# Kernel optimization log

Measured on AMD Instinct MI355X. Metric: run time of the kernel, lower is better.

The kernel has to match this reference:

```python
import jax, jax.numpy as jnp
import numpy as np

B, T_TREES, LEAVES = 1024, 34, 16
E = 128            # entity = logic = theorem embedding size
N_NF, N_LF = 4, 3  # binary numerical / logic function experts
V_ENT, V_TH = 2000, 32
GT_MAX, ENT_MAX, TH_MAX = 8, 16, 8


def setup_inputs() -> dict:
    key = jax.random.key(0)
    ks = jax.random.split(key, 24)
    s2e = 1.0 / np.sqrt(2 * E)
    s4e = 1.0 / np.sqrt(4 * E)
    se = 1.0 / np.sqrt(E)
    inp = {
        'leaf_idx': jax.random.randint(ks[0], (B, T_TREES, LEAVES), 0, V_ENT),
        'nf_ids':   jax.random.randint(ks[1], (B, T_TREES, 15), 0, N_NF),
        'lf_ids':   jax.random.randint(ks[2], (B, GT_MAX + 1), 0, N_LF),
        'th_idx':   jax.random.randint(ks[3], (B, TH_MAX), 0, V_TH),
        'ent_emb':  jax.random.normal(ks[4], (V_ENT, E)) * 0.02,
        'th_emb':   jax.random.normal(ks[5], (V_TH, E)) * 0.02,
        # nf two2one expert MLPs: Linear(2E,2E) -> ReLU -> Linear(2E,E)
        'nf_W1': jax.random.normal(ks[6], (N_NF, 2 * E, 2 * E)) * s2e,
        'nf_b1': jnp.zeros((N_NF, 2 * E)),
        'nf_W2': jax.random.normal(ks[7], (N_NF, 2 * E, E)) * s2e,
        'nf_b2': jnp.zeros((N_NF, E)),
        # lf two2one expert MLPs: Linear(2E,4E) -> ReLU -> Linear(4E,E)
        'lf_W1': jax.random.normal(ks[8], (N_LF, 2 * E, 4 * E)) * s2e,
        'lf_b1': jnp.zeros((N_LF, 4 * E)),
        'lf_W2': jax.random.normal(ks[9], (N_LF, 4 * E, E)) * s4e,
        'lf_b2': jnp.zeros((N_LF, E)),
        # higher attention linears: logic_size -> {entity,entity,theorem} size
        'he_W': jax.random.normal(ks[10], (E, E)) * se, 'he_b': jnp.zeros((E,)),
        'hg_W': jax.random.normal(ks[11], (E, E)) * se, 'hg_b': jnp.zeros((E,)),
        'ht_W': jax.random.normal(ks[12], (E, E)) * se, 'ht_b': jnp.zeros((E,)),
    }
    return inp


def _expert_mlp(x, ids, W1, b1, W2, b2):
    # x: [..., Din], ids: [...] selecting among K experts; masked sum over K (small fixed loop)
    out = jnp.zeros(x.shape[:-1] + (W2.shape[-1],), x.dtype)
    for k in range(W1.shape[0]):
        h = jax.nn.relu(x @ W1[k] + b1[k]) @ W2[k] + b2[k]
        out = out + jnp.where((ids == k)[..., None], h, 0.0)
    return out


def _attend(keys, q):
    # keys: [B, N, D], q: [B, D] -> attentive context [B, D]
    a = jax.nn.softmax(jnp.einsum('bnd,bd->bn', keys, q), axis=-1)
    return jnp.einsum('bn,bnd->bd', a, keys)


def _forward(leaf_idx, nf_ids, lf_ids, th_idx, ent_emb, th_emb,
             nf_W1, nf_b1, nf_W2, nf_b2, lf_W1, lf_b1, lf_W2, lf_b2,
             he_W, he_b, hg_W, hg_b, ht_W, ht_b):
    # leaf entity embedding lookup: [B, 34, 16, E]
    cur = ent_emb[leaf_idx]
    # recursive tree reduction over 4 levels of binary nf MLPs (batched over all nodes)
    off = 0
    for lvl in range(4):
        n = LEAVES >> (lvl + 1)  # nodes at this level: 8,4,2,1
        x = cur.reshape(cur.shape[0], T_TREES, n, 2 * E)  # concat(left,right)
        ids = nf_ids[..., off:off + n]
        off += n
        cur = _expert_mlp(x, ids, nf_W1, nf_b1, nf_W2, nf_b2)
    roots = cur[..., 0, :]                       # [B, 34, E]
    ent = roots[:, :ENT_MAX]                     # [B, 16, E] standalone entities
    pairs = roots[:, ENT_MAX:].reshape(roots.shape[0], GT_MAX + 1, 2 * E)
    stmt = _expert_mlp(pairs, lf_ids, lf_W1, lf_b1, lf_W2, lf_b2)  # [B, 9, E]
    gt = stmt[:, :GT_MAX]                        # [B, 8, E] ground truths
    obj = stmt[:, GT_MAX]                        # [B, E]    objective
    th = th_emb[th_idx]                          # [B, 8, E] theorems
    ent_ctx = _attend(ent, obj @ he_W + he_b)
    gt_ctx = _attend(gt, obj @ hg_W + hg_b)
    th_ctx = _attend(th, obj @ ht_W + ht_b)
    # higher attentive state: 2*L + E + T = 512
    return jnp.concatenate([obj, gt_ctx, ent_ctx, th_ctx], axis=-1)


def reference(leaf_idx, nf_ids, lf_ids, th_idx, ent_emb, th_emb,
              nf_W1, nf_b1, nf_W2, nf_b2, lf_W1, lf_b1, lf_W2, lf_b2,
              he_W, he_b, hg_W, hg_b, ht_W, ht_b):
    return _forward(leaf_idx, nf_ids, lf_ids, th_idx, ent_emb, th_emb,
                    nf_W1, nf_b1, nf_W2, nf_b2, lf_W1, lf_b1, lf_W2, lf_b2,
                    he_W, he_b, hg_W, hg_b, ht_W, ht_b)
```

## Files before the change

### kernel.cpp

```cpp
#include <hip/hip_runtime.h>
#include <math.h>


typedef unsigned short u16;
typedef unsigned int   u32;
typedef unsigned long long u64;
typedef __attribute__((ext_vector_type(8))) short v8s;
typedef __attribute__((ext_vector_type(4))) float f32x4;

__device__ __forceinline__ float b2f(u16 u) { return __uint_as_float(((u32)u) << 16); }
__device__ __forceinline__ u16 f2b(float f) {
  f = (f == f) ? f : 0.f;
  u32 x = __float_as_uint(f);
  u32 r = x + 0x7fffu + ((x >> 16) & 1u);
  return (u16)(r >> 16);
}

__device__ __forceinline__ void g2lds16(const void* g, void* l) {
  __builtin_amdgcn_global_load_lds(
      (const __attribute__((address_space(1))) void*)g,
      (__attribute__((address_space(3))) void*)l, 16, 0, 0);
}

#define NTREE 34816
#define RLEAF 9216

__global__ __launch_bounds__(256) void setup_k(
    const float* __restrict__ s0, const float* __restrict__ s1,
    const float* __restrict__ s2, const float* __restrict__ s3,
    const float* __restrict__ s4,
    u16* __restrict__ d0, u16* __restrict__ d1, u16* __restrict__ d2,
    u16* __restrict__ d3, u16* __restrict__ d4,
    const int* __restrict__ lf, int* __restrict__ leafcnt, int* __restrict__ leafperm,
    const int* __restrict__ nf, int* __restrict__ bh,
    const int CB, const int NB)
{
  __shared__ float tile[16][17];
  __shared__ int lcnt[16];
  const int t = threadIdx.x;
  const int bid = blockIdx.x;

  if (bid < 4840) {
    const int idx0 = bid * 256;
    if (idx0 < 983040) {
      const float* s; u16* d; int tb, estr, O, kt, mt, e;
      int tloc0;
      if (idx0 < 262144)      { s = s0; d = d0; tb = 0;      estr = 65536;  O = 256; }
      else if (idx0 < 393216) { s = s1; d = d1; tb = 262144; estr = 32768;  O = 128; }
      else if (idx0 < 786432) { s = s2; d = d2; tb = 393216; estr = 131072; O = 512; }
      else                    { s = s3; d = d3; tb = 786432; estr = 65536;  O = 128; }
      tloc0 = idx0 - tb;
      const int blk = tloc0 >> 9;
      const int hb  = (tloc0 >> 8) & 1;
      if (idx0 < 262144)      { kt = blk & 7;  mt = (blk >> 3) & 15; e = blk >> 7; }
      else if (idx0 < 393216) { kt = blk & 7;  mt = (blk >> 3) & 7;  e = blk >> 6; }
      else if (idx0 < 786432) { kt = blk & 7;  mt = (blk >> 3) & 31; e = blk >> 8; }
      else                    { kt = blk & 15; mt = (blk >> 4) & 7;  e = blk >> 7; }
      const int o0 = mt * 16;
      const int k0 = kt * 32 + hb * 16;
      tile[t >> 4][t & 15] = s[(size_t)e * estr + (size_t)(k0 + (t >> 4)) * O + o0 + (t & 15)];
      __syncthreads();
      d[tloc0 + t] = f2b(tile[((t >> 7) << 3) + (t & 7)][(t >> 3) & 15]);
    } else {
      int tl = idx0 + t - 983040;
      d4[tl] = f2b(s4[tl]);
    }
  } else if (bid < 4876) {
    const int gid = (bid - 4840) * 256 + t;
    const int id = lf[gid];
    const int lane = t & 63;
    for (int e = 0; e < 3; ++e) {
      u64 m = __ballot(id == e);
      if (!m) continue;
      int leader = __builtin_ctzll(m);
      int bp = 0;
      if (lane == leader) bp = atomicAdd(&leafcnt[e], (int)__popcll(m));
      bp = __shfl(bp, leader);
      if (id == e)
        leafperm[e * RLEAF + bp + (int)__popcll(m & ((1ull << lane) - 1ull))] = gid;
    }
  } else {
    const int hb2 = bid - 4876;
    const int c = hb2 / NB, b = hb2 - c * NB;
    const int bt0 = c * CB;
    int* bhc = bh + (size_t)c * 16 * NB;
    const int gid = b * 256 + t;
    int id = -1, lr = 0, cofs = 12, ioff = 14, shift = 0;
    if (gid < 8 * CB)       { lr = gid;          cofs = 0;  ioff = 0;  shift = 3; }
    else if (gid < 12 * CB) { lr = gid - 8*CB;   cofs = 4;  ioff = 8;  shift = 2; }
    else if (gid < 14 * CB) { lr = gid - 12*CB;  cofs = 8;  ioff = 12; shift = 1; }
    else if (gid < 15 * CB) { lr = gid - 14*CB;  }
    if (gid < 15 * CB) {
      int bt = bt0 + (lr >> shift);
      int n  = lr & ((1 << shift) - 1);
      id = nf[bt * 15 + ioff + n];
    }
    if (t < 16) lcnt[t] = 0;
    __syncthreads();
    const int lane = t & 63;
    #pragma unroll
    for (int e = 0; e < 4; ++e) {
      u64 m = __ballot(id == e);
      if (m && lane == __builtin_ctzll(m))
        atomicAdd(&lcnt[cofs + e], (int)__popcll(m));
    }
    __syncthreads();
    if (t < 16)
      bhc[t * NB + b] = lcnt[t];
  }
}

__global__ __launch_bounds__(1024) void perm_scan_k(
    int* __restrict__ bh, int* __restrict__ cnt, const int nb)
{
  const int c = blockIdx.x;
  int* bhc = bh + (size_t)c * 16 * nb;
  int* cntc = cnt + c * 16;
  const int s = threadIdx.x >> 6;
  const int lane = threadIdx.x & 63;
  int carry = 0;
  for (int b0 = 0; b0 < nb; b0 += 64) {
    const int b = b0 + lane;
    int v = (b < nb) ? bhc[s * nb + b] : 0;
    int x = v;
    #pragma unroll
    for (int d = 1; d < 64; d <<= 1) {
      int y = __shfl_up(x, d);
      if (lane >= d) x += y;
    }
    if (b < nb) bhc[s * nb + b] = carry + x - v;
    carry += __shfl(x, 63);
  }
  if (lane == 0) cntc[s] = carry;
}

__global__ __launch_bounds__(256) void perm_scatter_k(
    const int* __restrict__ nf, const int* __restrict__ bh,
    int* __restrict__ perm, const int CB, const int bt0, const int nb)
{
  const int gid = blockIdx.x * 256 + threadIdx.x;
  int id = -1, lr = 0, rows = CB, cofs = 12, pofs = 56 * CB, ioff = 14, shift = 0;
  if (gid < 8 * CB)       { lr = gid;          rows = 8*CB; cofs = 0;  pofs = 0;      ioff = 0;  shift = 3; }
  else if (gid < 12 * CB) { lr = gid - 8*CB;   rows = 4*CB; cofs = 4;  pofs = 32*CB;  ioff = 8;  shift = 2; }
  else if (gid < 14 * CB) { lr = gid - 12*CB;  rows = 2*CB; cofs = 8;  pofs = 48*CB;  ioff = 12; shift = 1; }
  else if (gid < 15 * CB) { lr = gid - 14*CB;                 }
  if (gid < 15 * CB) {
    int bt = bt0 + (lr >> shift);
    int n  = lr & ((1 << shift) - 1);
    id = nf[bt * 15 + ioff + n];
  }
  __shared__ int wc[4][16];
  const int w = threadIdx.x >> 6, lane = threadIdx.x & 63;
  if (lane < 16) wc[w][lane] = 0;
  __syncthreads();
  u64 msave[4];
  #pragma unroll
  for (int e = 0; e < 4; ++e) {
    u64 m = __ballot(id == e);
    msave[e] = m;
    if (m && lane == __builtin_ctzll(m))
      wc[w][cofs + e] = (int)__popcll(m);
  }
  __syncthreads();
  #pragma unroll
  for (int e = 0; e < 4; ++e) {
    if (id == e) {
      const int slot = cofs + e;
      int base = bh[slot * nb + blockIdx.x];
      #pragma unroll
      for (int w2 = 0; w2 < 3; ++w2)
        if (w2 < w) base += wc[w2][slot];
      perm[pofs + e * rows + base +
           (int)__popcll(msave[e] & ((1ull << lane) - 1ull))] = lr;
    }
  }
}

template<int HID, int NEXP, int MODE, int MR>
__global__ __launch_bounds__(256, 2) void mlp_k(
    const u16* __restrict__ src, const int* __restrict__ lidx,
    const u16* __restrict__ emb,
    const int* __restrict__ perm, const int* __restrict__ cnt,
    const int rows, const int bt0,
    const u16* __restrict__ W1f, const float* __restrict__ b1,
    const u16* __restrict__ W2f, const float* __restrict__ b2,
    u16* __restrict__ dst)
{
  constexpr int NT  = MR / 16;
  constexpr int MT1 = HID / 64;
  constexpr int K2  = HID / 32;
  constexpr int PD1 = (MT1 <= 4) ? 2 : 1;
  constexpr int NB1 = PD1 + 1;
  constexpr int XB  = MR * 512;
  constexpr int HB  = MR * HID * 2;
  constexpr int UB  = XB > HB ? XB : HB;
  __shared__ __align__(16) char uni[UB];
  __shared__ int rid[MR], soff[2 * MR];
  u16* const xs = (u16*)uni;
  u16* const hs = (u16*)uni;

  int bin = -1, tile = 0, cb = 0;
  {
    int rem = blockIdx.x;
    #pragma unroll
    for (int e = 0; e < NEXP; ++e) {
      int ce = cnt[e];
      int tt = (ce + MR - 1) / MR;
      if (bin < 0) {
        if (rem < tt) { bin = e; tile = rem; cb = ce; }
        else rem -= tt;
      }
    }
  }
  if (bin < 0) return;
  const int rbase = tile * MR;
  const int tid = threadIdx.x;
  const int w  = tid >> 6;
  const int lane = tid & 63;
  const int lm = lane & 15;
  const int lq = lane >> 4;

  const u16* const W1b = W1f + ((size_t)(bin * (HID / 16) + w * MT1) << 12) + lane * 8;
  const u16* const W2b = W2f + ((size_t)((bin * 8 + w * 2) * K2) << 9) + lane * 8;

  v8s afb[NB1][MT1];
  #pragma unroll
  for (int d = 0; d < PD1; ++d)
    #pragma unroll
    for (int m = 0; m < MT1; ++m)
      afb[d][m] = *(const v8s*)(W1b + (size_t)(m * 8 + d) * 512);

  if (tid < MR) {
    int rl = rbase + tid;
    int rlc = rl < cb ? rl : (cb - 1);
    rlc = rlc < 0 ? 0 : rlc;
    int rc = perm[(size_t)bin * rows + rlc];
    rc = rc < 0 ? 0 : (rc >= rows ? rows - 1 : rc);
    rid[tid] = (rl < cb) ? rc : -1;
    if (MODE == 0) {
      int bt = bt0 + (rc >> 3), node = rc & 7;
      int ia = lidx[bt * 16 + node * 2];
      int ib = lidx[bt * 16 + node * 2 + 1];
      ia = ia < 0 ? 0 : (ia > 1999 ? 1999 : ia);
      ib = ib < 0 ? 0 : (ib > 1999 ? 1999 : ib);
      soff[2 * tid]     = ia * 256;
      soff[2 * tid + 1] = ib * 256;
    } else {
      int base;
      if (MODE == 1) base = rc * 512;
      else { int bq = rc / 9, g = rc - bq * 9; base = (bq * 34 + 16 + 2 * g) * 256; }
      soff[2 * tid]     = base;
      soff[2 * tid + 1] = base + 256;
    }
  }
  __syncthreads();

  const char* const sb = (MODE == 0) ? (const char*)emb : (const char*)src;
  #pragma unroll
  for (int i = 0; i < MR / 8; ++i) {
    int d = i * 256 + tid;
    int r = d >> 5, c32d = d & 31;
    int cS = c32d ^ ((r & 7) << 1);
    const char* ga = sb + (size_t)(u32)soff[2 * r + (cS >> 4)] + (cS & 15) * 16;
    char* la = uni + ((size_t)(i * 256 + (tid & 192)) << 4);
    g2lds16(ga, la);
  }
  __syncthreads();

  int rdn[NT];
  #pragma unroll
  for (int n = 0; n < NT; ++n) rdn[n] = rid[n * 16 + lm];

  f32x4 acc[MT1][NT];
  #pragma unroll
  for (int m = 0; m < MT1; ++m)
    #pragma unroll
    for (int n = 0; n < NT; ++n)
      acc[m][n] = f32x4{0.f, 0.f, 0.f, 0.f};

  v8s bfr2[2][NT];
  #pragma unroll
  for (int n = 0; n < NT; ++n) {
    int r = n * 16 + lm;
    int cs = lq ^ ((lm & 7) << 1);
    bfr2[0][n] = *(const v8s*)(xs + r * 256 + cs * 8);
  }
  #pragma unroll
  for (int k = 0; k < 8; ++k) {
    const int cur = k % NB1;
    if (k + PD1 < 8) {
      const int nx = (k + PD1) % NB1;
      #pragma unroll
      for (int m = 0; m < MT1; ++m)
        afb[nx][m] = *(const v8s*)(W1b + (size_t)(m * 8 + k + PD1) * 512);
    }
    const int cb_ = k & 1;
    if (k < 7) {
      #pragma unroll
      for (int n = 0; n < NT; ++n) {
        int r = n * 16 + lm;
        int cs = ((k + 1) * 4 + lq) ^ ((lm & 7) << 1);
        bfr2[cb_ ^ 1][n] = *(const v8s*)(xs + r * 256 + cs * 8);
      }
    }
    __builtin_amdgcn_s_setprio(1);
    #pragma unroll
    for (int m = 0; m < MT1; ++m)
      #pragma unroll
      for (int n = 0; n < NT; ++n)
        acc[m][n] = __builtin_amdgcn_mfma_f32_16x16x32_bf16(afb[cur][m], bfr2[cb_][n], acc[m][n], 0, 0, 0);
    __builtin_amdgcn_s_setprio(0);
  }

  v8s afb2[3][2];
  #pragma unroll
  for (int m = 0; m < 2; ++m)
    afb2[0][m] = *(const v8s*)(W2b + (size_t)(m * K2) * 512);
  #pragma unroll
  for (int m = 0; m < 2; ++m)
    afb2[1][m] = *(const v8s*)(W2b + (size_t)(m * K2 + 1) * 512);

  __syncthreads();

  const float* b1b = b1 + bin * HID;
  #pragma unroll
  for (int m = 0; m < MT1; ++m) {
    const int f = (w * MT1 + m) * 16 + lq * 4;
    float bb0 = b1b[f], bb1 = b1b[f + 1], bb2 = b1b[f + 2], bb3 = b1b[f + 3];
    #pragma unroll
    for (int n = 0; n < NT; ++n) {
      union { u16 h[4]; uint2 v; } pk;
      f32x4 a = acc[m][n];
      pk.h[0] = f2b(fmaxf(a.x + bb0, 0.f));
      pk.h[1] = f2b(fmaxf(a.y + bb1, 0.f));
      pk.h[2] = f2b(fmaxf(a.z + bb2, 0.f));
      pk.h[3] = f2b(fmaxf(a.w + bb3, 0.f));
      int r = n * 16 + lm;
      int cs = (f >> 3) ^ ((lm & 7) << 1);
      *(uint2*)(uni + (size_t)r * (HID * 2) + (cs << 4) + (f & 7) * 2) = pk.v;
    }
  }
  __syncthreads();

  f32x4 acc2[2][NT];
  #pragma unroll
  for (int m = 0; m < 2; ++m)
    #pragma unroll
    for (int n = 0; n < NT; ++n)
      acc2[m][n] = f32x4{0.f, 0.f, 0.f, 0.f};

  #pragma unroll
  for (int n = 0; n < NT; ++n) {
    int r = n * 16 + lm;
    int cs = lq ^ ((lm & 7) << 1);
    bfr2[0][n] = *(const v8s*)(hs + (size_t)r * HID + cs * 8);
  }
  #pragma unroll
  for (int k = 0; k < K2; ++k) {
    const int cur = k % 3;
    if (k < K2 - 2) {
      const int nx2 = (k + 2) % 3;
      #pragma unroll
      for (int m = 0; m < 2; ++m)
        afb2[nx2][m] = *(const v8s*)(W2b + (size_t)(m * K2 + k + 2) * 512);
    }
    const int cb_ = k & 1;
    if (k < K2 - 1) {
      #pragma unroll
      for (int n = 0; n < NT; ++n) {
        int r = n * 16 + lm;
        int cs = ((k + 1) * 4 + lq) ^ ((lm & 7) << 1);
        bfr2[cb_ ^ 1][n] = *(const v8s*)(hs + (size_t)r * HID + cs * 8);
      }
    }
    __builtin_amdgcn_s_setprio(1);
    #pragma unroll
    for (int m = 0; m < 2; ++m)
      #pragma unroll
      for (int n = 0; n < NT; ++n)
        acc2[m][n] = __builtin_amdgcn_mfma_f32_16x16x32_bf16(afb2[cur][m], bfr2[cb_][n], acc2[m][n], 0, 0, 0);
    __builtin_amdgcn_s_setprio(0);
  }

  __syncthreads();
  const float* b2b = b2 + bin * 128;
  #pragma unroll
  for (int m = 0; m < 2; ++m) {
    const int f = (w * 2 + m) * 16 + lq * 4;
    float bb0 = b2b[f], bb1 = b2b[f + 1], bb2 = b2b[f + 2], bb3 = b2b[f + 3];
    #pragma unroll
    for (int n = 0; n < NT; ++n) {
      union { u16 h[4]; uint2 v; } pk;
      f32x4 a = acc2[m][n];
      pk.h[0] = f2b(a.x + bb0);
      pk.h[1] = f2b(a.y + bb1);
      pk.h[2] = f2b(a.z + bb2);
      pk.h[3] = f2b(a.w + bb3);
      int r = n * 16 + lm;
      int c = (w * 2 + m) * 2 + (lq >> 1);
      int cs = c ^ ((lm & 7) << 1);
      *(uint2*)(uni + r * 256 + cs * 16 + (lq & 1) * 8) = pk.v;
    }
  }
  __syncthreads();
  #pragma unroll
  for (int i = 0; i < MR / 16; ++i) {
    int cg = i * 256 + tid;
    int r = cg >> 4, sub = cg & 15;
    int rg = rid[r];
    if (rg >= 0) {
      uint4 v = *(const uint4*)(uni + r * 256 + ((sub ^ ((r & 7) << 1)) << 4));
      *(uint4*)((char*)dst + (size_t)rg * 256 + sub * 16) = v;
    }
  }
}

__global__ __launch_bounds__(128) void attn_k(
    const u16* __restrict__ stmt, const u16* __restrict__ roots,
    const float* __restrict__ themb, const int* __restrict__ thidx,
    const float* __restrict__ wHe, const float* __restrict__ bHe,
    const float* __restrict__ wHg, const float* __restrict__ bHg,
    const float* __restrict__ wHt, const float* __restrict__ bHt,
    float* __restrict__ out)
{
  const int b = blockIdx.x, t = threadIdx.x;
  __shared__ float obj_s[128], q_s[128], keys_s[16 * 132], a_s[16];

  const float obj = b2f(stmt[((size_t)b * 9 + 8) * 128 + t]);
  obj_s[t] = obj;
  out[(size_t)b * 512 + t] = obj;
  __syncthreads();

  for (int a = 0; a < 3; ++a) {
    int cntk;
    const float *Wt, *bv;
    if (a == 0) {
      cntk = 8; Wt = wHg; bv = bHg;
      for (int j = 0; j < 8; ++j)
        keys_s[j * 132 + t] = b2f(stmt[((size_t)b * 9 + j) * 128 + t]);
    } else if (a == 1) {
      cntk = 16; Wt = wHe; bv = bHe;
      for (int j = 0; j < 16; ++j)
        keys_s[j * 132 + t] = b2f(roots[((size_t)b * 34 + j) * 128 + t]);
    } else {
      cntk = 8; Wt = wHt; bv = bHt;
      for (int j = 0; j < 8; ++j) {
        int ti = thidx[b * 8 + j] & 31;
        keys_s[j * 132 + t] = themb[(size_t)ti * 128 + t];
      }
    }
    float q0 = 0.f, q1 = 0.f, q2 = 0.f, q3 = 0.f;
    #pragma unroll 4
    for (int k = 0; k < 128; k += 4) {
      q0 += obj_s[k]     * Wt[(k)     * 128 + t];
      q1 += obj_s[k + 1] * Wt[(k + 1) * 128 + t];
      q2 += obj_s[k + 2] * Wt[(k + 2) * 128 + t];
      q3 += obj_s[k + 3] * Wt[(k + 3) * 128 + t];
    }
    float qa = bv[t] + ((q0 + q1) + (q2 + q3));
    q_s[t] = (qa == qa) ? qa : 0.f;
    __syncthreads();
    {
      int j = t >> 3, s = t & 7;
      if (j < cntk) {
        float sc = 0.f;
        #pragma unroll
        for (int k = 0; k < 16; ++k)
          sc += keys_s[j * 132 + s * 16 + k] * q_s[s * 16 + k];
        sc += __shfl_xor(sc, 1);
        sc += __shfl_xor(sc, 2);
        sc += __shfl_xor(sc, 4);
        if (s == 0) a_s[j] = (sc == sc) ? sc : 0.f;
      }
    }
    __syncthreads();
    if (t < 16) {
      float v = (t < cntk) ? a_s[t] : -3.0e38f;
      float mx = v;
      #pragma unroll
      for (int d = 1; d < 16; d <<= 1) mx = fmaxf(mx, __shfl_xor(mx, d));
      float e = (t < cntk) ? expf(v - mx) : 0.f;
      float sm = e;
      #pragma unroll
      for (int d = 1; d < 16; d <<= 1) sm += __shfl_xor(sm, d);
      if (t < cntk) a_s[t] = e / sm;
    }
    __syncthreads();
    float c = 0.f;
    for (int j = 0; j < cntk; ++j) c += a_s[j] * keys_s[j * 132 + t];
    out[(size_t)b * 512 + 128 * (a + 1) + t] = c;
    __syncthreads();
  }
}

extern "C" void kernel_launch(void* const* d_in, const int* in_sizes, int n_in,
                              void* d_out, int out_size, void* d_ws, size_t ws_size,
                              hipStream_t stream)
{
  const int*   leaf_idx = (const int*)d_in[0];
  const int*   nf_ids   = (const int*)d_in[1];
  const int*   lf_ids   = (const int*)d_in[2];
  const int*   th_idx   = (const int*)d_in[3];
  const float* ent_emb  = (const float*)d_in[4];
  const float* th_emb   = (const float*)d_in[5];
  const float* nf_W1 = (const float*)d_in[6];
  const float* nf_b1 = (const float*)d_in[7];
  const float* nf_W2 = (const float*)d_in[8];
  const float* nf_b2 = (const float*)d_in[9];
  const float* lf_W1 = (const float*)d_in[10];
  const float* lf_b1 = (const float*)d_in[11];
  const float* lf_W2 = (const float*)d_in[12];
  const float* lf_b2 = (const float*)d_in[13];
  const float* he_W = (const float*)d_in[14];
  const float* he_b = (const float*)d_in[15];
  const float* hg_W = (const float*)d_in[16];
  const float* hg_b = (const float*)d_in[17];
  const float* ht_W = (const float*)d_in[18];
  const float* ht_b = (const float*)d_in[19];

  int CB = NTREE;
  while (CB > 544 && 14700000ull + (unsigned long long)CB * 3320ull > (unsigned long long)ws_size)
    CB >>= 1;
  const int nch = NTREE / CB;
  const int NB = (15 * CB + 255) / 256;

  char* ws = (char*)d_ws;
  size_t off = 0;
  auto take = [&](size_t bytes) -> char* {
    char* p = ws + off;
    off = (off + bytes + 255) & ~(size_t)255;
    return p;
  };
  int* cnt      = (int*)take(8192);
  int* leafperm = (int*)take((size_t)3 * RLEAF * 4);
  int* chperm   = (int*)take((size_t)60 * CB * 4);
  int* bh       = (int*)take((size_t)nch * 16 * NB * 4);
  u16* wN1  = (u16*)take((size_t)4 * 256 * 256 * 2);
  u16* wN2  = (u16*)take((size_t)4 * 128 * 256 * 2);
  u16* wL1  = (u16*)take((size_t)3 * 512 * 256 * 2);
  u16* wL2  = (u16*)take((size_t)3 * 128 * 512 * 2);
  u16* embB = (u16*)take((size_t)2000 * 128 * 2);
  u16* bufA  = (u16*)take((size_t)CB * 8 * 128 * 2);
  u16* bufB  = (u16*)take((size_t)CB * 4 * 128 * 2);
  u16* roots = (u16*)take((size_t)NTREE * 128 * 2);
  u16* stmt  = (u16*)take((size_t)RLEAF * 128 * 2);

  int* leafcnt = cnt + nch * 16;

  hipMemsetAsync(leafcnt, 0, 8 * 4, stream);
  setup_k<<<4876 + nch * NB, 256, 0, stream>>>(
      nf_W1, nf_W2, lf_W1, lf_W2, ent_emb, wN1, wN2, wL1, wL2, embB,
      lf_ids, leafcnt, leafperm, nf_ids, bh, CB, NB);
  perm_scan_k<<<nch, 1024, 0, stream>>>(bh, cnt, NB);

  for (int c = 0; c < nch; ++c) {
    const int bt0 = c * CB;
    int* ccnt = cnt + c * 16;
    perm_scatter_k<<<NB, 256, 0, stream>>>(nf_ids, bh + (size_t)c * 16 * NB,
                                           chperm, CB, bt0, NB);
    mlp_k<256, 4, 0, 96><<<(8 * CB + 95) / 96 + 4, 256, 0, stream>>>(
        nullptr, leaf_idx, embB, chperm, ccnt, 8 * CB, bt0,
        wN1, nf_b1, wN2, nf_b2, bufA);
    mlp_k<256, 4, 1, 96><<<(4 * CB + 95) / 96 + 4, 256, 0, stream>>>(
        bufA, nullptr, nullptr, chperm + 32 * CB, ccnt + 4, 4 * CB, 0,
        wN1, nf_b1, wN2, nf_b2, bufB);
    mlp_k<256, 4, 1, 64><<<(2 * CB + 63) / 64 + 4, 256, 0, stream>>>(
        bufB, nullptr, nullptr, chperm + 48 * CB, ccnt + 8, 2 * CB, 0,
        wN1, nf_b1, wN2, nf_b2, bufA);
    mlp_k<256, 4, 1, 64><<<(CB + 63) / 64 + 4, 256, 0, stream>>>(
        bufA, nullptr, nullptr, chperm + 56 * CB, ccnt + 12, CB, 0,
        wN1, nf_b1, wN2, nf_b2, roots + (size_t)bt0 * 128);
  }

  mlp_k<512, 3, 2, 32><<<RLEAF / 32 + 3, 256, 0, stream>>>(
      roots, nullptr, nullptr, leafperm, leafcnt, RLEAF, 0,
      wL1, lf_b1, wL2, lf_b2, stmt);

  attn_k<<<1024, 128, 0, stream>>>(stmt, roots, th_emb, th_idx,
                                   he_W, he_b, hg_W, hg_b, ht_W, ht_b,
                                   (float*)d_out);
}
```

Before: 296.8 us.

## Fuse scatter, tree MLP levels, logic MLP and attention into persistent kernel

Replaces the per-chunk sequence of scatter, four tree-level MLP launches, the logic MLP and the attention launch with one persistent kernel. Blocks loop over virtual block indices and synchronise through a hierarchical atomic grid barrier in workspace memory. The aim is to remove the launch gaps and tail idling between many small dependent kernels. In exchange it relies on every block being co-resident, costs spin-wait overhead at each barrier, and fixes LDS usage at the largest stage's size, which may lower occupancy.

```diff
diff --git a/kernel.cpp b/kernel.cpp
--- a/kernel.cpp
+++ b/kernel.cpp
@@ -20,6 +20,33 @@
   __builtin_amdgcn_global_load_lds(
       (const __attribute__((address_space(1))) void*)g,
       (__attribute__((address_space(3))) void*)l, 16, 0, 0);
+}
+
+__device__ __forceinline__ void gbar(int* gb, int nblk) {
+  __syncthreads();
+  if (threadIdx.x == 0) {
+    __threadfence();
+    int g = __hip_atomic_load(gb + 272, __ATOMIC_ACQUIRE, __HIP_MEMORY_SCOPE_AGENT);
+    const int grp = blockIdx.x & 15;
+    const int gsz = (nblk >> 4) + (grp < (nblk & 15) ? 1 : 0);
+    int a = __hip_atomic_fetch_add(gb + grp * 16, 1, __ATOMIC_ACQ_REL, __HIP_MEMORY_SCOPE_AGENT);
+    if (a == gsz - 1) {
+      __hip_atomic_store(gb + grp * 16, 0, __ATOMIC_RELAXED, __HIP_MEMORY_SCOPE_AGENT);
+      int r = __hip_atomic_fetch_add(gb + 256, 1, __ATOMIC_ACQ_REL, __HIP_MEMORY_SCOPE_AGENT);
+      if (r == 15) {
+        __hip_atomic_store(gb + 256, 0, __ATOMIC_RELAXED, __HIP_MEMORY_SCOPE_AGENT);
+        __hip_atomic_fetch_add(gb + 272, 1, __ATOMIC_RELEASE, __HIP_MEMORY_SCOPE_AGENT);
+      } else {
+        while (__hip_atomic_load(gb + 272, __ATOMIC_ACQUIRE, __HIP_MEMORY_SCOPE_AGENT) == g)
+          __builtin_amdgcn_s_sleep(16);
+      }
+    } else {
+      while (__hip_atomic_load(gb + 272, __ATOMIC_ACQUIRE, __HIP_MEMORY_SCOPE_AGENT) == g)
+        __builtin_amdgcn_s_sleep(16);
+    }
+    __threadfence();
+  }
+  __syncthreads();
 }
 
 #define NTREE 34816
@@ -134,24 +161,25 @@
   if (lane == 0) cntc[s] = carry;
 }
 
-__global__ __launch_bounds__(256) void perm_scatter_k(
-    const int* __restrict__ nf, const int* __restrict__ bh,
-    int* __restrict__ perm, const int CB, const int bt0, const int nb)
+
+__device__ void scatter_body(int vb, const int* __restrict__ nf,
+    const int* __restrict__ bh, int* __restrict__ perm,
+    const int CB, const int bt0, const int nb, int* wc)
 {
-  const int gid = blockIdx.x * 256 + threadIdx.x;
+  __syncthreads();
+  const int gid = vb * 256 + threadIdx.x;
   int id = -1, lr = 0, rows = CB, cofs = 12, pofs = 56 * CB, ioff = 14, shift = 0;
   if (gid < 8 * CB)       { lr = gid;          rows = 8*CB; cofs = 0;  pofs = 0;      ioff = 0;  shift = 3; }
   else if (gid < 12 * CB) { lr = gid - 8*CB;   rows = 4*CB; cofs = 4;  pofs = 32*CB;  ioff = 8;  shift = 2; }
   else if (gid < 14 * CB) { lr = gid - 12*CB;  rows = 2*CB; cofs = 8;  pofs = 48*CB;  ioff = 12; shift = 1; }
-  else if (gid < 15 * CB) { lr = gid - 14*CB;                 }
+  else if (gid < 15 * CB) { lr = gid - 14*CB;  }
   if (gid < 15 * CB) {
     int bt = bt0 + (lr >> shift);
     int n  = lr & ((1 << shift) - 1);
     id = nf[bt * 15 + ioff + n];
   }
-  __shared__ int wc[4][16];
   const int w = threadIdx.x >> 6, lane = threadIdx.x & 63;
-  if (lane < 16) wc[w][lane] = 0;
+  if (lane < 16) wc[w * 16 + lane] = 0;
   __syncthreads();
   u64 msave[4];
   #pragma unroll
@@ -159,17 +187,17 @@
     u64 m = __ballot(id == e);
     msave[e] = m;
     if (m && lane == __builtin_ctzll(m))
-      wc[w][cofs + e] = (int)__popcll(m);
+      wc[w * 16 + cofs + e] = (int)__popcll(m);
   }
   __syncthreads();
   #pragma unroll
   for (int e = 0; e < 4; ++e) {
     if (id == e) {
       const int slot = cofs + e;
-      int base = bh[slot * nb + blockIdx.x];
+      int base = bh[slot * nb + vb];
       #pragma unroll
       for (int w2 = 0; w2 < 3; ++w2)
-        if (w2 < w) base += wc[w2][slot];
+        if (w2 < w) base += wc[w2 * 16 + slot];
       perm[pofs + e * rows + base +
            (int)__popcll(msave[e] & ((1ull << lane) - 1ull))] = lr;
     }
@@ -177,31 +205,28 @@
 }
 
 template<int HID, int NEXP, int MODE, int MR>
-__global__ __launch_bounds__(256, 2) void mlp_k(
+__device__ void mlp_body(int vb,
     const u16* __restrict__ src, const int* __restrict__ lidx,
     const u16* __restrict__ emb,
     const int* __restrict__ perm, const int* __restrict__ cnt,
     const int rows, const int bt0,
     const u16* __restrict__ W1f, const float* __restrict__ b1,
     const u16* __restrict__ W2f, const float* __restrict__ b2,
-    u16* __restrict__ dst)
+    u16* __restrict__ dst, char* uni, int* rid, int* soff)
 {
   constexpr int NT  = MR / 16;
   constexpr int MT1 = HID / 64;
   constexpr int K2  = HID / 32;
   constexpr int PD1 = (MT1 <= 4) ? 2 : 1;
   constexpr int NB1 = PD1 + 1;
-  constexpr int XB  = MR * 512;
-  constexpr int HB  = MR * HID * 2;
-  constexpr int UB  = XB > HB ? XB : HB;
-  __shared__ __align__(16) char uni[UB];
-  __shared__ int rid[MR], soff[2 * MR];
   u16* const xs = (u16*)uni;
   u16* const hs = (u16*)uni;
 
+  __syncthreads();
+
   int bin = -1, tile = 0, cb = 0;
   {
-    int rem = blockIdx.x;
+    int rem = vb;
     #pragma unroll
     for (int e = 0; e < NEXP; ++e) {
       int ce = cnt[e];
@@ -270,6 +295,7 @@
   int rdn[NT];
   #pragma unroll
   for (int n = 0; n < NT; ++n) rdn[n] = rid[n * 16 + lm];
+  (void)rdn;
 
   f32x4 acc[MT1][NT];
   #pragma unroll
@@ -415,7 +441,7 @@
   }
 }
 
-__global__ __launch_bounds__(128) void attn_k(
+__device__ void attn_body(int vb, char* uni,
     const u16* __restrict__ stmt, const u16* __restrict__ roots,
     const float* __restrict__ themb, const int* __restrict__ thidx,
     const float* __restrict__ wHe, const float* __restrict__ bHe,
@@ -423,12 +449,18 @@
     const float* __restrict__ wHt, const float* __restrict__ bHt,
     float* __restrict__ out)
 {
-  const int b = blockIdx.x, t = threadIdx.x;
-  __shared__ float obj_s[128], q_s[128], keys_s[16 * 132], a_s[16];
-
-  const float obj = b2f(stmt[((size_t)b * 9 + 8) * 128 + t]);
-  obj_s[t] = obj;
-  out[(size_t)b * 512 + t] = obj;
+  __syncthreads();
+  const int t = threadIdx.x;
+  const int h = t >> 7, tl = t & 127;
+  const int b = vb * 2 + h;
+  float* obj_s  = (float*)uni + h * 128;
+  float* q_s    = (float*)(uni + 1024) + h * 128;
+  float* keys_s = (float*)(uni + 2048) + h * 2112;
+  float* a_s    = (float*)(uni + 18944) + h * 16;
+
+  const float obj = b2f(stmt[((size_t)b * 9 + 8) * 128 + tl]);
+  obj_s[tl] = obj;
+  out[(size_t)b * 512 + tl] = obj;
   __syncthreads();
 
   for (int a = 0; a < 3; ++a) {
@@ -437,31 +469,31 @@
     if (a == 0) {
       cntk = 8; Wt = wHg; bv = bHg;
       for (int j = 0; j < 8; ++j)
-        keys_s[j * 132 + t] = b2f(stmt[((size_t)b * 9 + j) * 128 + t]);
+        keys_s[j * 132 + tl] = b2f(stmt[((size_t)b * 9 + j) * 128 + tl]);
     } else if (a == 1) {
       cntk = 16; Wt = wHe; bv = bHe;
       for (int j = 0; j < 16; ++j)
-        keys_s[j * 132 + t] = b2f(roots[((size_t)b * 34 + j) * 128 + t]);
+        keys_s[j * 132 + tl] = b2f(roots[((size_t)b * 34 + j) * 128 + tl]);
     } else {
       cntk = 8; Wt = wHt; bv = bHt;
       for (int j = 0; j < 8; ++j) {
         int ti = thidx[b * 8 + j] & 31;
-        keys_s[j * 132 + t] = themb[(size_t)ti * 128 + t];
+        keys_s[j * 132 + tl] = themb[(size_t)ti * 128 + tl];
       }
     }
     float q0 = 0.f, q1 = 0.f, q2 = 0.f, q3 = 0.f;
     #pragma unroll 4
     for (int k = 0; k < 128; k += 4) {
-      q0 += obj_s[k]     * Wt[(k)     * 128 + t];
-      q1 += obj_s[k + 1] * Wt[(k + 1) * 128 + t];
-      q2 += obj_s[k + 2] * Wt[(k + 2) * 128 + t];
-      q3 += obj_s[k + 3] * Wt[(k + 3) * 128 + t];
-    }
-    float qa = bv[t] + ((q0 + q1) + (q2 + q3));
-    q_s[t] = (qa == qa) ? qa : 0.f;
+      q0 += obj_s[k]     * Wt[(k)     * 128 + tl];
+      q1 += obj_s[k + 1] * Wt[(k + 1) * 128 + tl];
+      q2 += obj_s[k + 2] * Wt[(k + 2) * 128 + tl];
+      q3 += obj_s[k + 3] * Wt[(k + 3) * 128 + tl];
+    }
+    float qa = bv[tl] + ((q0 + q1) + (q2 + q3));
+    q_s[tl] = (qa == qa) ? qa : 0.f;
     __syncthreads();
     {
-      int j = t >> 3, s = t & 7;
+      int j = tl >> 3, s = tl & 7;
       if (j < cntk) {
         float sc = 0.f;
         #pragma unroll
@@ -474,23 +506,92 @@
       }
     }
     __syncthreads();
-    if (t < 16) {
-      float v = (t < cntk) ? a_s[t] : -3.0e38f;
+    if (tl < 16) {
+      float v = (tl < cntk) ? a_s[tl] : -3.0e38f;
       float mx = v;
       #pragma unroll
       for (int d = 1; d < 16; d <<= 1) mx = fmaxf(mx, __shfl_xor(mx, d));
-      float e = (t < cntk) ? expf(v - mx) : 0.f;
+      float e = (tl < cntk) ? expf(v - mx) : 0.f;
       float sm = e;
       #pragma unroll
       for (int d = 1; d < 16; d <<= 1) sm += __shfl_xor(sm, d);
-      if (t < cntk) a_s[t] = e / sm;
+      if (tl < cntk) a_s[tl] = e / sm;
     }
     __syncthreads();
     float c = 0.f;
-    for (int j = 0; j < cntk; ++j) c += a_s[j] * keys_s[j * 132 + t];
-    out[(size_t)b * 512 + 128 * (a + 1) + t] = c;
+    for (int j = 0; j < cntk; ++j) c += a_s[j] * keys_s[j * 132 + tl];
+    out[(size_t)b * 512 + 128 * (a + 1) + tl] = c;
     __syncthreads();
   }
+}
+
+__global__ __launch_bounds__(256, 2) void chain_k(
+    const int* __restrict__ nf, const int* __restrict__ bh,
+    int* __restrict__ chperm, const int* __restrict__ cnt,
+    const int* __restrict__ lidx, const u16* __restrict__ embB,
+    const u16* __restrict__ wN1, const float* __restrict__ nb1,
+    const u16* __restrict__ wN2, const float* __restrict__ nb2,
+    const u16* __restrict__ wL1, const float* __restrict__ lb1,
+    const u16* __restrict__ wL2, const float* __restrict__ lb2,
+    u16* __restrict__ bufA, u16* __restrict__ bufB,
+    u16* __restrict__ roots, u16* __restrict__ stmt,
+    const int* __restrict__ leafperm, const int* __restrict__ leafcnt,
+    const float* __restrict__ themb, const int* __restrict__ thidx,
+    const float* __restrict__ wHe, const float* __restrict__ bHe,
+    const float* __restrict__ wHg, const float* __restrict__ bHg,
+    const float* __restrict__ wHt, const float* __restrict__ bHt,
+    float* __restrict__ out, int* __restrict__ gb,
+    const int CB, const int NB, const int nch)
+{
+  __shared__ __align__(16) char uni[49152];
+  __shared__ int rid_s[96], soff_s[192], wc_s[64];
+  const int NBLK = gridDim.x;
+  const int bid = blockIdx.x;
+
+  for (int c = 0; c < nch; ++c) {
+    const int bt0 = c * CB;
+    const int* ccnt = cnt + c * 16;
+    const int* bhc = bh + (size_t)c * 16 * NB;
+
+    for (int vb = bid; vb < NB; vb += NBLK)
+      scatter_body(vb, nf, bhc, chperm, CB, bt0, NB, wc_s);
+    gbar(gb, NBLK);
+
+    int n0 = (8 * CB + 95) / 96 + 4;
+    for (int vb = bid; vb < n0; vb += NBLK)
+      mlp_body<256, 4, 0, 96>(vb, nullptr, lidx, embB, chperm, ccnt, 8 * CB, bt0,
+                              wN1, nb1, wN2, nb2, bufA, uni, rid_s, soff_s);
+    gbar(gb, NBLK);
+
+    int n1 = (4 * CB + 95) / 96 + 4;
+    for (int vb = bid; vb < n1; vb += NBLK)
+      mlp_body<256, 4, 1, 96>(vb, bufA, nullptr, nullptr, chperm + 32 * CB, ccnt + 4,
+                              4 * CB, 0, wN1, nb1, wN2, nb2, bufB, uni, rid_s, soff_s);
+    gbar(gb, NBLK);
+
+    int n2 = (2 * CB + 63) / 64 + 4;
+    for (int vb = bid; vb < n2; vb += NBLK)
+      mlp_body<256, 4, 1, 64>(vb, bufB, nullptr, nullptr, chperm + 48 * CB, ccnt + 8,
+                              2 * CB, 0, wN1, nb1, wN2, nb2, bufA, uni, rid_s, soff_s);
+    gbar(gb, NBLK);
+
+    int n3 = (CB + 63) / 64 + 4;
+    for (int vb = bid; vb < n3; vb += NBLK)
+      mlp_body<256, 4, 1, 64>(vb, bufA, nullptr, nullptr, chperm + 56 * CB, ccnt + 12,
+                              CB, 0, wN1, nb1, wN2, nb2,
+                              roots + (size_t)bt0 * 128, uni, rid_s, soff_s);
+    gbar(gb, NBLK);
+  }
+
+  int nl = RLEAF / 32 + 3;
+  for (int vb = bid; vb < nl; vb += NBLK)
+    mlp_body<512, 3, 2, 32>(vb, roots, nullptr, nullptr, leafperm, leafcnt,
+                            RLEAF, 0, wL1, lb1, wL2, lb2, stmt, uni, rid_s, soff_s);
+  gbar(gb, NBLK);
+
+  for (int vb = bid; vb < 512; vb += NBLK)
+    attn_body(vb, uni, stmt, roots, themb, thidx,
+              wHe, bHe, wHg, bHg, wHt, bHt, out);
 }
 
 extern "C" void kernel_launch(void* const* d_in, const int* in_sizes, int n_in,
@@ -532,6 +633,7 @@
     return p;
   };
   int* cnt      = (int*)take(8192);
+  int* gb       = (int*)take(2048);
   int* leafperm = (int*)take((size_t)3 * RLEAF * 4);
   int* chperm   = (int*)take((size_t)60 * CB * 4);
   int* bh       = (int*)take((size_t)nch * 16 * NB * 4);
@@ -547,36 +649,23 @@
 
   int* leafcnt = cnt + nch * 16;
 
-  hipMemsetAsync(leafcnt, 0, 8 * 4, stream);
+  hipMemsetAsync(cnt, 0, 8192 + 2048, stream);
+
   setup_k<<<4876 + nch * NB, 256, 0, stream>>>(
       nf_W1, nf_W2, lf_W1, lf_W2, ent_emb, wN1, wN2, wL1, wL2, embB,
       lf_ids, leafcnt, leafperm, nf_ids, bh, CB, NB);
   perm_scan_k<<<nch, 1024, 0, stream>>>(bh, cnt, NB);
 
-  for (int c = 0; c < nch; ++c) {
-    const int bt0 = c * CB;
-    int* ccnt = cnt + c * 16;
-    perm_scatter_k<<<NB, 256, 0, stream>>>(nf_ids, bh + (size_t)c * 16 * NB,
-                                           chperm, CB, bt0, NB);
-    mlp_k<256, 4, 0, 96><<<(8 * CB + 95) / 96 + 4, 256, 0, stream>>>(
-        nullptr, leaf_idx, embB, chperm, ccnt, 8 * CB, bt0,
-        wN1, nf_b1, wN2, nf_b2, bufA);
-    mlp_k<256, 4, 1, 96><<<(4 * CB + 95) / 96 + 4, 256, 0, stream>>>(
-        bufA, nullptr, nullptr, chperm + 32 * CB, ccnt + 4, 4 * CB, 0,
-        wN1, nf_b1, wN2, nf_b2, bufB);
-    mlp_k<256, 4, 1, 64><<<(2 * CB + 63) / 64 + 4, 256, 0, stream>>>(
-        bufB, nullptr, nullptr, chperm + 48 * CB, ccnt + 8, 2 * CB, 0,
-        wN1, nf_b1, wN2, nf_b2, bufA);
-    mlp_k<256, 4, 1, 64><<<(CB + 63) / 64 + 4, 256, 0, stream>>>(
-        bufA, nullptr, nullptr, chperm + 56 * CB, ccnt + 12, CB, 0,
-        wN1, nf_b1, wN2, nf_b2, roots + (size_t)bt0 * 128);
-  }
-
-  mlp_k<512, 3, 2, 32><<<RLEAF / 32 + 3, 256, 0, stream>>>(
-      roots, nullptr, nullptr, leafperm, leafcnt, RLEAF, 0,
-      wL1, lf_b1, wL2, lf_b2, stmt);
-
-  attn_k<<<1024, 128, 0, stream>>>(stmt, roots, th_emb, th_idx,
-                                   he_W, he_b, hg_W, hg_b, ht_W, ht_b,
-                                   (float*)d_out);
-}
+  int occ = 0;
+  hipOccupancyMaxActiveBlocksPerMultiprocessor(&occ, chain_k, 256, 0);
+  if (occ < 1) occ = 1;
+  if (occ > 3) occ = 3;
+  const int NBLK = occ * 256;
+
+  chain_k<<<NBLK, 256, 0, stream>>>(
+      nf_ids, bh, chperm, cnt, leaf_idx, embB,
+      wN1, nf_b1, wN2, nf_b2, wL1, lf_b1, wL2, lf_b2,
+      bufA, bufB, roots, stmt, leafperm, leafcnt,
+      th_emb, th_idx, he_W, he_b, hg_W, hg_b, ht_W, ht_b,
+      (float*)d_out, gb, CB, NB, nch);
+}
```

Measured after the change: 743.0 us. 2.5x slower.
